# Kernel tuning notes

Hardware: AMD Instinct MI355X
Metric: run time of the kernel (lower is better)

The kernel has to match this reference:

```python
import jax, jax.numpy as jnp
import numpy as np

EMBED_DIM = 768
NUM_HEADS = 12


def setup_inputs() -> dict:
    key = jax.random.key(0)
    k_x, k_w1, k_b1, k_w2, k_b2 = jax.random.split(key, 5)
    B, S, D = 4, 2048, EMBED_DIM
    s1 = 1.0 / np.sqrt(D)
    return {
        "x": jax.random.normal(k_x, (B, S, D), dtype=jnp.float32),
        "W1": jax.random.uniform(k_w1, (D, 3 * D), jnp.float32, -s1, s1),  # proj1 weight (in,out)
        "b1": jax.random.uniform(k_b1, (3 * D,), jnp.float32, -s1, s1),
        "W2": jax.random.uniform(k_w2, (D, D), jnp.float32, -s1, s1),  # proj2 weight (in,out)
        "b2": jax.random.uniform(k_b2, (D,), jnp.float32, -s1, s1),
    }


def reference(x, W1, b1, W2, b2):
    B, S, D = x.shape
    H = NUM_HEADS
    h = D // H
    qkv = x @ W1 + b1                       # [B,S,3D]
    qkv = qkv.reshape(B, S, H, 3 * h).transpose(0, 2, 1, 3)  # [B,H,S,3h]
    # chunk order in the original: K, Q, V
    K = qkv[..., :h]
    Q = qkv[..., h:2 * h]
    V = qkv[..., 2 * h:]
    # NOTE: original code computes Q @ V^T (not Q @ K^T) -- reproduced faithfully
    scores = jnp.einsum("bhqd,bhkd->bhqk", Q, V) / jnp.sqrt(jnp.float32(h))
    att = jax.nn.softmax(scores, axis=-1)
    out = jnp.einsum("bhqk,bhkd->bhqd", att, V)  # [B,H,S,h]
    out = out.transpose(0, 2, 1, 3).reshape(B, S, D)
    return out @ W2 + b2
```

## Files before the change

kernel.cpp:

```cpp
#include <hip/hip_runtime.h>
#include <hip/hip_bf16.h>
#include <math.h>


#define SEQ   2048
#define DIM   768
#define NHEAD 12
#define HDIM  64
#define BATCH 4

#define QSCALE 0.1803368801111244f

typedef __attribute__((ext_vector_type(8))) short s16x8;
typedef __attribute__((ext_vector_type(4))) float f32x4;

#if __has_builtin(__builtin_amdgcn_exp2f)
#define EXP2F(x) __builtin_amdgcn_exp2f(x)
#else
#define EXP2F(x) exp2f(x)
#endif

__device__ __forceinline__ unsigned short f2bf(float f) {
    union { float f; unsigned int u; } v; v.f = f;
    unsigned int r = v.u + 0x7fffu + ((v.u >> 16) & 1u);
    return (unsigned short)(r >> 16);
}

__device__ __forceinline__ unsigned int cvt_pk_bf16(float a, float b) {
    unsigned int r;
    asm("v_cvt_pk_bf16_f32 %0, %1, %2" : "=v"(r) : "v"(a), "v"(b));
    return r;
}

__device__ __forceinline__ void gload_lds16(const void* g, void* l) {
    __builtin_amdgcn_global_load_lds(
        (const __attribute__((address_space(1))) unsigned int*)g,
        (__attribute__((address_space(3))) unsigned int*)l, 16, 0, 0);
}

__global__ __launch_bounds__(256) void cvt_all(
    const float* __restrict__ x, const float* __restrict__ W1,
    const float* __restrict__ W2, unsigned short* __restrict__ xb,
    unsigned short* __restrict__ W1bt, unsigned short* __restrict__ W2bt)
{
    __shared__ float T[32][33];
    const int id = blockIdx.x;

    if (id >= 1728) {
        const size_t i4 = ((size_t)(id - 1728) * 256 + threadIdx.x) * 4;
        float4 v = *(const float4*)&x[i4];
        ushort4 o;
        o.x = f2bf(v.x); o.y = f2bf(v.y); o.z = f2bf(v.z); o.w = f2bf(v.w);
        *(ushort4*)&xb[i4] = o;
        return;
    }

    const float* W;
    unsigned short* out;
    int n0, k0, src_ld, c0;
    if (id < 1152) {
        W = W1; out = W1bt; src_ld = 2304;
        n0 = (id % 48) * 32; k0 = (id / 48) * 32;
        c0 = (n0 >> 7) * 192 + 64 + (n0 & 127);
    } else {
        const int id2 = id - 1152;
        W = W2; out = W2bt; src_ld = DIM;
        n0 = (id2 % 24) * 32; k0 = (id2 / 24) * 32;
        c0 = n0;
    }
    const int tc = threadIdx.x & 31, tr = threadIdx.x >> 5;
    #pragma unroll
    for (int i = 0; i < 4; ++i)
        T[tr + i * 8][tc] = W[(size_t)(k0 + tr + i * 8) * src_ld + c0 + tc];
    __syncthreads();
    #pragma unroll
    for (int i = 0; i < 4; ++i)
        out[(size_t)(n0 + tr + i * 8) * DIM + k0 + tc] = f2bf(T[tc][tr + i * 8]);
}

__device__ __forceinline__ void gemm128_loop(
    const unsigned short* __restrict__ A, const unsigned short* __restrict__ B,
    unsigned short* As, unsigned short* Bs, int m0, int n0, f32x4 acc[4][4])
{
    const int tid  = threadIdx.x;
    const int wave = tid >> 6;
    const int lane = tid & 63;
    const int quad = lane >> 4;
    const int lcol = lane & 15;
    const int wm = wave >> 1, wn = wave & 1;

    const int sr = lane >> 2;
    const int sp = lane & 3;
    const int sc = sp ^ ((sr >> 1) & 3);

    const int aswz = ((quad ^ ((lcol >> 1) & 3)) << 4);

    for (int k0 = 0; k0 < DIM; k0 += 32) {
        #pragma unroll
        for (int s = 0; s < 2; ++s) {
            const int r0 = wave * 32 + s * 16;
            gload_lds16(&A[(size_t)(m0 + r0 + sr) * DIM + k0 + sc * 8],
                        (void*)&As[r0 * 32]);
            gload_lds16(&B[(size_t)(n0 + r0 + sr) * DIM + k0 + sc * 8],
                        (void*)&Bs[r0 * 32]);
        }
        __syncthreads();

        s16x8 af[4], bf[4];
        #pragma unroll
        for (int mt = 0; mt < 4; ++mt) {
            const int row = wm * 64 + mt * 16 + lcol;
            af[mt] = *(const s16x8*)((const char*)As + row * 64 + aswz);
        }
        #pragma unroll
        for (int nt = 0; nt < 4; ++nt) {
            const int row = wn * 64 + nt * 16 + lcol;
            bf[nt] = *(const s16x8*)((const char*)Bs + row * 64 + aswz);
        }
        #pragma unroll
        for (int mt = 0; mt < 4; ++mt)
            #pragma unroll
            for (int nt = 0; nt < 4; ++nt)
                acc[mt][nt] = __builtin_amdgcn_mfma_f32_16x16x32_bf16(
                    af[mt], bf[nt], acc[mt][nt], 0, 0, 0);
        __syncthreads();
    }
}

__global__ __launch_bounds__(256) void qkv_gemm_bf16(
    const unsigned short* __restrict__ xb, const unsigned short* __restrict__ W1bt,
    const float* __restrict__ b1, unsigned short* __restrict__ Qb,
    unsigned short* __restrict__ Vr, unsigned short* __restrict__ Vt)
{
    __shared__ unsigned short LDSBUF[8192];
    f32x4 acc[4][4] = {};
    const int id  = blockIdx.y * 12 + blockIdx.x;
    const int swz = (id & 7) * 96 + (id >> 3);
    const int m0 = (swz / 12) * 128, n0 = (swz % 12) * 128;
    gemm128_loop(xb, W1bt, LDSBUF, LDSBUF + 4096, m0, n0, acc);

    const int tid  = threadIdx.x;
    const int wave = tid >> 6, lane = tid & 63;
    const int quad = lane >> 4, lcol = lane & 15;
    const int wm = wave >> 1, wn = wave & 1;

    const int colblock = n0 + wn * 64;
    const int head = colblock >> 7;
    const int cc0  = colblock & 127;
    const int isQ  = (cc0 == 0);
    const float scale = isQ ? QSCALE : 1.0f;
    unsigned short* dst = isQ ? Qb : Vr;

    float bias[4];
    #pragma unroll
    for (int nt = 0; nt < 4; ++nt)
        bias[nt] = b1[head * 192 + 64 + cc0 + nt * 16 + lcol];

    unsigned short* Wst = LDSBUF + wave * 2048;

    #pragma unroll
    for (int half = 0; half < 2; ++half) {
        #pragma unroll
        for (int mh = 0; mh < 2; ++mh) {
            const int mt = half * 2 + mh;
            #pragma unroll
            for (int nt = 0; nt < 4; ++nt)
                #pragma unroll
                for (int r = 0; r < 4; ++r) {
                    const float v = (acc[mt][nt][r] + bias[nt]) * scale;
                    Wst[(mh * 16 + quad * 4 + r) * 64 + nt * 16 + lcol] = f2bf(v);
                }
        }
        __syncthreads();
        #pragma unroll
        for (int p = 0; p < 4; ++p) {
            const int lr = p * 8 + (lane >> 3);
            const int c8 = (lane & 7) * 8;
            s16x8 v = *(const s16x8*)&Wst[lr * 64 + c8];
            const int m  = m0 + wm * 64 + half * 32 + lr;
            const int bb = m >> 11;
            const int s  = m & 2047;
            const int bhh = bb * NHEAD + head;
            *(s16x8*)&dst[((size_t)bhh * SEQ + s) * HDIM + c8] = v;
        }
        __syncthreads();
    }

    if (!isQ) {
        #pragma unroll
        for (int nt = 0; nt < 4; ++nt) {
            const int d = nt * 16 + lcol;
            #pragma unroll
            for (int mt = 0; mt < 4; ++mt) {
                const int m0r = m0 + wm * 64 + mt * 16 + quad * 4;
                const int bb  = m0r >> 11;
                const int s0  = m0r & 2047;
                const int bhh = bb * NHEAD + head;
                ushort4 o;
                o.x = f2bf(acc[mt][nt][0] + bias[nt]);
                o.y = f2bf(acc[mt][nt][1] + bias[nt]);
                o.z = f2bf(acc[mt][nt][2] + bias[nt]);
                o.w = f2bf(acc[mt][nt][3] + bias[nt]);
                *(ushort4*)&Vt[((size_t)bhh * HDIM + d) * SEQ + s0] = o;
            }
        }
    }
}

__global__ __launch_bounds__(256) void attn_mfma(
    const unsigned short* __restrict__ Qb, const unsigned short* __restrict__ Vr,
    const unsigned short* __restrict__ Vt, unsigned short* __restrict__ Yb)
{
    __shared__ unsigned short VrS[2][64 * 64];
    __shared__ unsigned short VtS[2][64 * 64];
    __shared__ unsigned short Ps[4][32 * 72];

    const int bh = blockIdx.x;
    const int b  = bh / NHEAD;
    const int hh = bh % NHEAD;
    const int q0 = blockIdx.y * 128;

    const int tid  = threadIdx.x;
    const int wave = tid >> 6;
    const int lane = tid & 63;
    const int quad = lane >> 4;
    const int lcol = lane & 15;

    s16x8 qa[2][2];
    #pragma unroll
    for (int mt = 0; mt < 2; ++mt)
        #pragma unroll
        for (int kk = 0; kk < 2; ++kk)
            qa[mt][kk] = *(const s16x8*)&Qb[((size_t)bh * SEQ + q0 + wave * 32 + mt * 16 + lcol) * HDIM
                                            + kk * 32 + quad * 8];

    s16x8 ones;
    #pragma unroll
    for (int i = 0; i < 8; ++i) ones[i] = (short)0x3F80;

    f32x4 oacc[2][4] = {};
    f32x4 lsum[2] = {};

    const int srow = lane >> 3;
    const int schk = (lane & 7) ^ srow;

    s16x8 rv[2], rt[2];
    #pragma unroll
    for (int s = 0; s < 2; ++s) {
        const int r0 = wave * 16 + s * 8;
        rv[s] = *(const s16x8*)&Vr[((size_t)bh * SEQ + r0 + srow) * HDIM + schk * 8];
        rt[s] = *(const s16x8*)&Vt[((size_t)bh * HDIM + r0 + srow) * SEQ + schk * 8];
    }
    #pragma unroll
    for (int s = 0; s < 2; ++s) {
        const int r0 = wave * 16 + s * 8;
        *(s16x8*)((char*)&VrS[0][r0 * 64] + lane * 16) = rv[s];
        *(s16x8*)((char*)&VtS[0][r0 * 64] + lane * 16) = rt[s];
    }
    __syncthreads();

    int cur = 0;
    for (int k0 = 0; k0 < SEQ; k0 += 64) {
        const bool more = (k0 + 64 < SEQ);
        if (more) {
            #pragma unroll
            for (int s = 0; s < 2; ++s) {
                const int r0 = wave * 16 + s * 8;
                rv[s] = *(const s16x8*)&Vr[((size_t)bh * SEQ + k0 + 64 + r0 + srow) * HDIM + schk * 8];
                rt[s] = *(const s16x8*)&Vt[((size_t)bh * HDIM + r0 + srow) * SEQ + k0 + 64 + schk * 8];
            }
            __builtin_amdgcn_sched_barrier(0);
        }

        const unsigned short* VrC = &VrS[cur][0];
        const unsigned short* VtC = &VtS[cur][0];

        f32x4 sT[4][2] = {};
        #pragma unroll
        for (int kk = 0; kk < 2; ++kk) {
            s16x8 af[4];
            #pragma unroll
            for (int kt = 0; kt < 4; ++kt) {
                const int r = kt * 16 + lcol;
                const int c = kk * 4 + quad;
                af[kt] = *(const s16x8*)((const char*)VrC + r * 128 + ((c ^ (r & 7)) << 4));
            }
            #pragma unroll
            for (int kt = 0; kt < 4; ++kt)
                #pragma unroll
                for (int mt = 0; mt < 2; ++mt)
                    sT[kt][mt] = __builtin_amdgcn_mfma_f32_16x16x32_bf16(
                        af[kt], qa[mt][kk], sT[kt][mt], 0, 0, 0);
        }

        #pragma unroll
        for (int kt = 0; kt < 4; ++kt)
            #pragma unroll
            for (int mt = 0; mt < 2; ++mt) {
                const float p0 = EXP2F(sT[kt][mt][0]);
                const float p1 = EXP2F(sT[kt][mt][1]);
                const float p2 = EXP2F(sT[kt][mt][2]);
                const float p3 = EXP2F(sT[kt][mt][3]);
                uint2 w;
                w.x = cvt_pk_bf16(p0, p1);
                w.y = cvt_pk_bf16(p2, p3);
                *(uint2*)&Ps[wave][(mt * 16 + lcol) * 72 + kt * 16 + quad * 4] = w;
            }

        #pragma unroll
        for (int kk = 0; kk < 2; ++kk) {
            s16x8 pa[2];
            #pragma unroll
            for (int mt = 0; mt < 2; ++mt)
                pa[mt] = *(const s16x8*)&Ps[wave][(mt * 16 + lcol) * 72 + kk * 32 + quad * 8];
            #pragma unroll
            for (int mt = 0; mt < 2; ++mt)
                lsum[mt] = __builtin_amdgcn_mfma_f32_16x16x32_bf16(
                    pa[mt], ones, lsum[mt], 0, 0, 0);
            #pragma unroll
            for (int dt = 0; dt < 4; ++dt) {
                const int r = dt * 16 + lcol;
                const int c = kk * 4 + quad;
                s16x8 vb = *(const s16x8*)((const char*)VtC + r * 128 + ((c ^ (r & 7)) << 4));
                #pragma unroll
                for (int mt = 0; mt < 2; ++mt)
                    oacc[mt][dt] = __builtin_amdgcn_mfma_f32_16x16x32_bf16(
                        pa[mt], vb, oacc[mt][dt], 0, 0, 0);
            }
        }

        if (more) {
            const int nb = cur ^ 1;
            #pragma unroll
            for (int s = 0; s < 2; ++s) {
                const int r0 = wave * 16 + s * 8;
                *(s16x8*)((char*)&VrS[nb][r0 * 64] + lane * 16) = rv[s];
                *(s16x8*)((char*)&VtS[nb][r0 * 64] + lane * 16) = rt[s];
            }
        }
        __syncthreads();
        cur ^= 1;
    }

    #pragma unroll
    for (int mt = 0; mt < 2; ++mt)
        #pragma unroll
        for (int r = 0; r < 4; ++r) {
            const float invl = 1.0f / lsum[mt][r];
            const int qrow = q0 + wave * 32 + mt * 16 + quad * 4 + r;
            #pragma unroll
            for (int dt = 0; dt < 4; ++dt)
                Yb[((size_t)b * SEQ + qrow) * DIM + hh * HDIM + dt * 16 + lcol] =
                    f2bf(oacc[mt][dt][r] * invl);
        }
}

__global__ __launch_bounds__(256) void proj_gemm_bf16(
    const unsigned short* __restrict__ Yb, const unsigned short* __restrict__ W2bt,
    const float* __restrict__ b2, float* __restrict__ out)
{
    __shared__ unsigned short LDSBUF[8192];
    unsigned short* As = LDSBUF;
    unsigned short* Bs = LDSBUF + 2048;

    const int tid  = threadIdx.x;
    const int wave = tid >> 6;
    const int lane = tid & 63;
    const int quad = lane >> 4;
    const int lcol = lane & 15;
    const int wm = wave >> 1, wn = wave & 1;

    const int id  = blockIdx.y * 6 + blockIdx.x;
    const int swz = (id & 7) * 96 + (id >> 3);
    const int m0 = (swz / 6) * 64, n0 = (swz % 6) * 128;

    const int sr = lane >> 2;
    const int sp = lane & 3;
    const int sc = sp ^ ((sr >> 1) & 3);
    const int aswz = ((quad ^ ((lcol >> 1) & 3)) << 4);

    f32x4 acc[2][4] = {};

    for (int k0 = 0; k0 < DIM; k0 += 32) {
        {
            const int r0 = wave * 16;
            gload_lds16(&Yb[(size_t)(m0 + r0 + sr) * DIM + k0 + sc * 8],
                        (void*)&As[r0 * 32]);
        }
        #pragma unroll
        for (int s = 0; s < 2; ++s) {
            const int r0 = wave * 32 + s * 16;
            gload_lds16(&W2bt[(size_t)(n0 + r0 + sr) * DIM + k0 + sc * 8],
                        (void*)&Bs[r0 * 32]);
        }
        __syncthreads();

        s16x8 af[2], bf[4];
        #pragma unroll
        for (int mt = 0; mt < 2; ++mt) {
            const int row = wm * 32 + mt * 16 + lcol;
            af[mt] = *(const s16x8*)((const char*)As + row * 64 + aswz);
        }
        #pragma unroll
        for (int nt = 0; nt < 4; ++nt) {
            const int row = wn * 64 + nt * 16 + lcol;
            bf[nt] = *(const s16x8*)((const char*)Bs + row * 64 + aswz);
        }
        #pragma unroll
        for (int mt = 0; mt < 2; ++mt)
            #pragma unroll
            for (int nt = 0; nt < 4; ++nt)
                acc[mt][nt] = __builtin_amdgcn_mfma_f32_16x16x32_bf16(
                    af[mt], bf[nt], acc[mt][nt], 0, 0, 0);
        __syncthreads();
    }

    float bias[4];
    #pragma unroll
    for (int nt = 0; nt < 4; ++nt)
        bias[nt] = b2[n0 + wn * 64 + nt * 16 + lcol];

    float* W32 = (float*)LDSBUF + wave * 1024;

    #pragma unroll
    for (int mt = 0; mt < 2; ++mt) {
        #pragma unroll
        for (int nt = 0; nt < 4; ++nt)
            #pragma unroll
            for (int r = 0; r < 4; ++r)
                W32[(quad * 4 + r) * 64 + nt * 16 + lcol] = acc[mt][nt][r] + bias[nt];
        __syncthreads();
        #pragma unroll
        for (int p = 0; p < 4; ++p) {
            const int lr = p * 4 + (lane >> 4);
            float4 v = *(const float4*)&W32[lr * 64 + (lane & 15) * 4];
            const int m = m0 + wm * 32 + mt * 16 + lr;
            *(float4*)&out[(size_t)m * DIM + n0 + wn * 64 + (lane & 15) * 4] = v;
        }
        __syncthreads();
    }
}

extern "C" void kernel_launch(void* const* d_in, const int* in_sizes, int n_in,
                              void* d_out, int out_size, void* d_ws, size_t ws_size,
                              hipStream_t stream)
{
    const float* x  = (const float*)d_in[0];
    const float* W1 = (const float*)d_in[1];
    const float* b1 = (const float*)d_in[2];
    const float* W2 = (const float*)d_in[3];
    const float* b2 = (const float*)d_in[4];
    float* out = (float*)d_out;

    const size_t NQV = (size_t)BATCH * NHEAD * SEQ * HDIM;
    unsigned short* Qb   = (unsigned short*)d_ws;
    unsigned short* Vr   = Qb + NQV;
    unsigned short* Vt   = Vr + NQV;
    unsigned short* Yb   = Vt + NQV;
    unsigned short* xb   = Yb + NQV;
    unsigned short* W1bt = xb + NQV;
    unsigned short* W2bt = W1bt + 1536 * DIM;

    cvt_all<<<7872, 256, 0, stream>>>(x, W1, W2, xb, W1bt, W2bt);

    qkv_gemm_bf16<<<dim3(12, 64), 256, 0, stream>>>(xb, W1bt, b1, Qb, Vr, Vt);
    attn_mfma<<<dim3(BATCH * NHEAD, SEQ / 128), 256, 0, stream>>>(Qb, Vr, Vt, Yb);
    proj_gemm_bf16<<<dim3(DIM / 128, 128), 256, 0, stream>>>(Yb, W2bt, b2, out);
}
```

Measured before the change: 204.9 us.

## Double-buffer LDS in QKV GEMM with register-staged prefetch

Replaces the direct global-to-LDS loads in the QKV projection GEMM with a double-buffered scheme. The next K-slice is loaded into registers while MFMAs run on the current LDS buffer, then written to the alternate buffer, leaving one barrier per iteration instead of two. This aims to hide global load latency behind compute, at the cost of twice the LDS, extra VGPRs, and an extra register-to-LDS write step.

```diff
diff --git a/kernel.cpp b/kernel.cpp
--- a/kernel.cpp
+++ b/kernel.cpp
@@ -78,9 +78,9 @@
         out[(size_t)(n0 + tr + i * 8) * DIM + k0 + tc] = f2bf(T[tc][tr + i * 8]);
 }
 
-__device__ __forceinline__ void gemm128_loop(
+__device__ __forceinline__ void gemm128_loop_dbuf(
     const unsigned short* __restrict__ A, const unsigned short* __restrict__ B,
-    unsigned short* As, unsigned short* Bs, int m0, int n0, f32x4 acc[4][4])
+    unsigned short* L, int m0, int n0, f32x4 acc[4][4])
 {
     const int tid  = threadIdx.x;
     const int wave = tid >> 6;
@@ -95,27 +95,47 @@
 
     const int aswz = ((quad ^ ((lcol >> 1) & 3)) << 4);
 
+    s16x8 ra[2], rb[2];
+    #pragma unroll
+    for (int s = 0; s < 2; ++s) {
+        const int r0 = wave * 32 + s * 16;
+        ra[s] = *(const s16x8*)&A[(size_t)(m0 + r0 + sr) * DIM + sc * 8];
+        rb[s] = *(const s16x8*)&B[(size_t)(n0 + r0 + sr) * DIM + sc * 8];
+    }
+    #pragma unroll
+    for (int s = 0; s < 2; ++s) {
+        const int r0 = wave * 32 + s * 16;
+        *(s16x8*)((char*)(L + r0 * 32) + lane * 16) = ra[s];
+        *(s16x8*)((char*)(L + 8192 + r0 * 32) + lane * 16) = rb[s];
+    }
+    __syncthreads();
+
+    int cur = 0;
     for (int k0 = 0; k0 < DIM; k0 += 32) {
-        #pragma unroll
-        for (int s = 0; s < 2; ++s) {
-            const int r0 = wave * 32 + s * 16;
-            gload_lds16(&A[(size_t)(m0 + r0 + sr) * DIM + k0 + sc * 8],
-                        (void*)&As[r0 * 32]);
-            gload_lds16(&B[(size_t)(n0 + r0 + sr) * DIM + k0 + sc * 8],
-                        (void*)&Bs[r0 * 32]);
-        }
-        __syncthreads();
+        const bool more = (k0 + 32 < DIM);
+        if (more) {
+            #pragma unroll
+            for (int s = 0; s < 2; ++s) {
+                const int r0 = wave * 32 + s * 16;
+                ra[s] = *(const s16x8*)&A[(size_t)(m0 + r0 + sr) * DIM + k0 + 32 + sc * 8];
+                rb[s] = *(const s16x8*)&B[(size_t)(n0 + r0 + sr) * DIM + k0 + 32 + sc * 8];
+            }
+            __builtin_amdgcn_sched_barrier(0);
+        }
+
+        const unsigned short* AsC = L + cur * 4096;
+        const unsigned short* BsC = L + 8192 + cur * 4096;
 
         s16x8 af[4], bf[4];
         #pragma unroll
         for (int mt = 0; mt < 4; ++mt) {
             const int row = wm * 64 + mt * 16 + lcol;
-            af[mt] = *(const s16x8*)((const char*)As + row * 64 + aswz);
+            af[mt] = *(const s16x8*)((const char*)AsC + row * 64 + aswz);
         }
         #pragma unroll
         for (int nt = 0; nt < 4; ++nt) {
             const int row = wn * 64 + nt * 16 + lcol;
-            bf[nt] = *(const s16x8*)((const char*)Bs + row * 64 + aswz);
+            bf[nt] = *(const s16x8*)((const char*)BsC + row * 64 + aswz);
         }
         #pragma unroll
         for (int mt = 0; mt < 4; ++mt)
@@ -123,7 +143,18 @@
             for (int nt = 0; nt < 4; ++nt)
                 acc[mt][nt] = __builtin_amdgcn_mfma_f32_16x16x32_bf16(
                     af[mt], bf[nt], acc[mt][nt], 0, 0, 0);
-        __syncthreads();
+
+        if (more) {
+            const int nb = cur ^ 1;
+            #pragma unroll
+            for (int s = 0; s < 2; ++s) {
+                const int r0 = wave * 32 + s * 16;
+                *(s16x8*)((char*)(L + nb * 4096 + r0 * 32) + lane * 16) = ra[s];
+                *(s16x8*)((char*)(L + 8192 + nb * 4096 + r0 * 32) + lane * 16) = rb[s];
+            }
+        }
+        __syncthreads();
+        cur ^= 1;
     }
 }
 
@@ -132,12 +163,12 @@
     const float* __restrict__ b1, unsigned short* __restrict__ Qb,
     unsigned short* __restrict__ Vr, unsigned short* __restrict__ Vt)
 {
-    __shared__ unsigned short LDSBUF[8192];
+    __shared__ unsigned short LDSBUF[16384];
     f32x4 acc[4][4] = {};
     const int id  = blockIdx.y * 12 + blockIdx.x;
     const int swz = (id & 7) * 96 + (id >> 3);
     const int m0 = (swz / 12) * 128, n0 = (swz % 12) * 128;
-    gemm128_loop(xb, W1bt, LDSBUF, LDSBUF + 4096, m0, n0, acc);
+    gemm128_loop_dbuf(xb, W1bt, LDSBUF, m0, n0, acc);
 
     const int tid  = threadIdx.x;
     const int wave = tid >> 6, lane = tid & 63;
```

Measured after the change: 198.9 us. 3.0% less time.
